# Kernel optimization log

Hardware: AMD Instinct MI355X
Metric: run time of the kernel (lower is better)

Reference implementation:

```python
import jax, jax.numpy as jnp
import numpy as np

V, C, T, H, L, B = 32000, 1024, 1024, 16, 4, 4
HD = C // H
FF = 4 * C
LN_EPS = 1e-5


def _sinusoidal(block_size, n_embd):
    pos = np.arange(block_size, dtype=np.float32)[:, None]
    div = np.exp(np.arange(0, n_embd, 2, dtype=np.float32) * (-np.log(10000.0) / n_embd))
    enc = np.zeros((block_size, n_embd), dtype=np.float32)
    enc[:, 0::2] = np.sin(pos * div)
    enc[:, 1::2] = np.cos(pos * div)
    return jnp.asarray(enc)


def setup_inputs() -> dict:
    key = jax.random.key(0)
    ks = jax.random.split(key, 12)
    std = 0.02
    n = lambda k, s: jax.random.normal(k, s, jnp.float32) * std
    return {
        'idx': jax.random.randint(ks[0], (B, T), 0, V),
        'emb': n(ks[1], (V, C)),
        'pos_enc': _sinusoidal(T, C),
        'Wq': n(ks[2], (L, C, C)),
        'Wk': n(ks[3], (L, C, C)),
        'Wv': n(ks[4], (L, C, C)),
        'Wo': n(ks[5], (L, C, C)),
        'bo': jnp.zeros((L, C), jnp.float32),
        'W1': n(ks[6], (L, C, FF)),
        'b1': jnp.zeros((L, FF), jnp.float32),
        'W2': n(ks[7], (L, FF, C)),
        'b2': jnp.zeros((L, C), jnp.float32),
        'ln1_g': jnp.ones((L, C), jnp.float32),
        'ln1_b': jnp.zeros((L, C), jnp.float32),
        'ln2_g': jnp.ones((L, C), jnp.float32),
        'ln2_b': jnp.zeros((L, C), jnp.float32),
        'lnf_g': jnp.ones((C,), jnp.float32),
        'lnf_b': jnp.zeros((C,), jnp.float32),
        'Wlm': n(ks[8], (C, V)),
        'blm': jnp.zeros((V,), jnp.float32),
    }


def _layer_norm(x, g, b):
    m = jnp.mean(x, -1, keepdims=True)
    v = jnp.var(x, -1, keepdims=True)
    return (x - m) * jax.lax.rsqrt(v + LN_EPS) * g + b


def _forward(idx, emb, pos_enc, Wq, Wk, Wv, Wo, bo, W1, b1, W2, b2,
             ln1_g, ln1_b, ln2_g, ln2_b, lnf_g, lnf_b, Wlm, blm):
    Bv, Tv = idx.shape
    x = emb[idx] + pos_enc[None, :Tv, :]  # [B,T,C]
    mask = jnp.tril(jnp.ones((Tv, Tv), dtype=bool))
    scale = HD ** -0.5

    def block(x, p):
        wq, wk, wv, wo, bov, w1, b1v, w2, b2v, g1, bn1, g2, bn2 = p
        h = _layer_norm(x, g1, bn1)
        q = jnp.einsum('btc,chd->bhtd', h, wq.reshape(C, H, HD))
        k = jnp.einsum('btc,chd->bhtd', h, wk.reshape(C, H, HD))
        v = jnp.einsum('btc,chd->bhtd', h, wv.reshape(C, H, HD))
        wei = jnp.einsum('bhqd,bhkd->bhqk', q, k) * scale
        wei = jnp.where(mask, wei, -jnp.inf)
        wei = jax.nn.softmax(wei, axis=-1)
        o = jnp.einsum('bhqk,bhkd->bhqd', wei, v)
        o = o.transpose(0, 2, 1, 3).reshape(Bv, Tv, C)
        x = x + o @ wo + bov
        h2 = _layer_norm(x, g2, bn2)
        x = x + jax.nn.gelu(h2 @ w1 + b1v, approximate=False) @ w2 + b2v
        return x, None

    x, _ = jax.lax.scan(block, x, (Wq, Wk, Wv, Wo, bo, W1, b1, W2, b2,
                                   ln1_g, ln1_b, ln2_g, ln2_b))
    x = _layer_norm(x, lnf_g, lnf_b)
    return x @ Wlm + blm  # [B,T,V]


def reference(idx, emb, pos_enc, Wq, Wk, Wv, Wo, bo, W1, b1, W2, b2,
              ln1_g, ln1_b, ln2_g, ln2_b, lnf_g, lnf_b, Wlm, blm):
    return _forward(idx, emb, pos_enc, Wq, Wk, Wv, Wo, bo, W1, b1, W2, b2,
                    ln1_g, ln1_b, ln2_g, ln2_b, lnf_g, lnf_b, Wlm, blm)
```

## Files before the change

kernel.cpp:

```cpp
#include <hip/hip_runtime.h>

#define V_  32000
#define C_  1024
#define T_  1024
#define H_  16
#define L_  4
#define B_  4
#define HD_ 64
#define FF_ 4096
#define M_  (B_ * T_)

typedef __attribute__((ext_vector_type(8))) short bf16x8;
typedef __attribute__((ext_vector_type(4))) float f32x4;
typedef unsigned short u16;

#define FENCE() asm volatile("" ::: "memory")
#define BAR()  do { FENCE(); __builtin_amdgcn_s_barrier(); FENCE(); } while (0)
#define VMW(n) asm volatile("s_waitcnt vmcnt(" #n ")" ::: "memory")

__device__ __forceinline__ u16 f2bf(float f) {
  unsigned u = __builtin_bit_cast(unsigned, f);
  u += 0x7fffu + ((u >> 16) & 1u);
  return (u16)(u >> 16);
}

__device__ __forceinline__ float gelu_f(float v) {
  return 0.5f * v * (1.0f + erff(v * 0.70710678118654752f));
}

__device__ __forceinline__ void gload16(const u16* g, u16* l) {
  __builtin_amdgcn_global_load_lds(
      (const __attribute__((address_space(1))) void*)g,
      (__attribute__((address_space(3))) void*)l, 16, 0, 0);
}

template <int FUSE_LN>
__global__ __launch_bounds__(256)
void embed_kernel(const int* __restrict__ idx, const float* __restrict__ emb,
                  const float* __restrict__ pos, float* __restrict__ x,
                  const float* __restrict__ g, const float* __restrict__ bta,
                  u16* __restrict__ hout) {
  int row = blockIdx.x;
  int t = row & (T_ - 1);
  int tok = idx[row];
  float4 e = reinterpret_cast<const float4*>(emb + (size_t)tok * C_)[threadIdx.x];
  float4 p = reinterpret_cast<const float4*>(pos + (size_t)t * C_)[threadIdx.x];
  float4 r;
  r.x = e.x + p.x; r.y = e.y + p.y; r.z = e.z + p.z; r.w = e.w + p.w;
  reinterpret_cast<float4*>(x + (size_t)row * C_)[threadIdx.x] = r;
  if constexpr (FUSE_LN) {
    int tid = threadIdx.x;
    float s  = r.x + r.y + r.z + r.w;
    float ss = r.x * r.x + r.y * r.y + r.z * r.z + r.w * r.w;
    #pragma unroll
    for (int d = 1; d < 64; d <<= 1) {
      s  += __shfl_xor(s, d, 64);
      ss += __shfl_xor(ss, d, 64);
    }
    __shared__ float rs[4], rss[4];
    int w = tid >> 6, lane = tid & 63;
    if (lane == 0) { rs[w] = s; rss[w] = ss; }
    __syncthreads();
    s  = rs[0] + rs[1] + rs[2] + rs[3];
    ss = rss[0] + rss[1] + rss[2] + rss[3];
    float mean = s * (1.0f / C_);
    float var  = ss * (1.0f / C_) - mean * mean;
    float rstd = rsqrtf(var + 1e-5f);
    float4 gv = reinterpret_cast<const float4*>(g)[tid];
    float4 bv = reinterpret_cast<const float4*>(bta)[tid];
    union { u16 u[4]; uint2 v; } pk;
    pk.u[0] = f2bf((r.x - mean) * rstd * gv.x + bv.x);
    pk.u[1] = f2bf((r.y - mean) * rstd * gv.y + bv.y);
    pk.u[2] = f2bf((r.z - mean) * rstd * gv.z + bv.z);
    pk.u[3] = f2bf((r.w - mean) * rstd * gv.w + bv.w);
    *reinterpret_cast<uint2*>(&hout[(size_t)row * C_ + tid * 4]) = pk.v;
  }
}

__global__ __launch_bounds__(256)
void ln_kernel(const float* __restrict__ xin, const float* __restrict__ g,
               const float* __restrict__ bta, u16* __restrict__ out) {
  const int w = threadIdx.x >> 6, lane = threadIdx.x & 63;
  const int row = blockIdx.x * 4 + w;
  const float4* xr = reinterpret_cast<const float4*>(xin + (size_t)row * C_);
  float4 xv[4];
  float s = 0.f, ss = 0.f;
  #pragma unroll
  for (int j = 0; j < 4; ++j) {
    xv[j] = xr[lane + 64 * j];
    s  += xv[j].x + xv[j].y + xv[j].z + xv[j].w;
    ss += xv[j].x * xv[j].x + xv[j].y * xv[j].y + xv[j].z * xv[j].z + xv[j].w * xv[j].w;
  }
  #pragma unroll
  for (int d = 1; d < 64; d <<= 1) {
    s  += __shfl_xor(s, d, 64);
    ss += __shfl_xor(ss, d, 64);
  }
  float mean = s * (1.0f / C_);
  float var  = ss * (1.0f / C_) - mean * mean;
  float rstd = rsqrtf(var + 1e-5f);
  #pragma unroll
  for (int j = 0; j < 4; ++j) {
    float4 gv = reinterpret_cast<const float4*>(g)[lane + 64 * j];
    float4 bv = reinterpret_cast<const float4*>(bta)[lane + 64 * j];
    union { u16 u[4]; uint2 v; } pk;
    pk.u[0] = f2bf((xv[j].x - mean) * rstd * gv.x + bv.x);
    pk.u[1] = f2bf((xv[j].y - mean) * rstd * gv.y + bv.y);
    pk.u[2] = f2bf((xv[j].z - mean) * rstd * gv.z + bv.z);
    pk.u[3] = f2bf((xv[j].w - mean) * rstd * gv.w + bv.w);
    *reinterpret_cast<uint2*>(&out[(size_t)row * C_ + (lane + 64 * j) * 4]) = pk.v;
  }
}

__global__ __launch_bounds__(256)
void wtrans_kernel(const float* __restrict__ W, u16* __restrict__ Wt, int K, int N,
                   size_t dstBS) {
  const float* src = W + (size_t)blockIdx.z * K * N;
  u16* dst = Wt + (size_t)blockIdx.z * dstBS;
  __shared__ float tile[32][33];
  int k0 = blockIdx.y * 32, n0 = blockIdx.x * 32;
  int tx = threadIdx.x & 31, ty = threadIdx.x >> 5;
  #pragma unroll
  for (int i = 0; i < 4; ++i)
    tile[ty * 4 + i][tx] = src[(size_t)(k0 + ty * 4 + i) * N + n0 + tx];
  __syncthreads();
  int n = threadIdx.x >> 3, q = threadIdx.x & 7;
  union { u16 u[4]; uint2 v; } pk;
  #pragma unroll
  for (int j = 0; j < 4; ++j) pk.u[j] = f2bf(tile[4 * q + j][n]);
  *reinterpret_cast<uint2*>(&dst[(size_t)(n0 + n) * K + k0 + 4 * q]) = pk.v;
}

__global__ __launch_bounds__(256)
void wtrans4_kernel(const float* __restrict__ Wq, const float* __restrict__ Wk,
                    const float* __restrict__ Wv, const float* __restrict__ Wo,
                    u16* __restrict__ WqkvT, u16* __restrict__ WoT) {
  int zz = blockIdx.z;
  int l = zz & 3, which = zz >> 2;
  const float* src = (which == 0 ? Wq : which == 1 ? Wk : which == 2 ? Wv : Wo)
                     + (size_t)l * C_ * C_;
  u16* dst = (which == 3)
      ? WoT + (size_t)l * C_ * C_
      : WqkvT + (size_t)l * 3 * C_ * C_ + (size_t)which * C_ * C_;
  __shared__ float tile[32][33];
  int k0 = blockIdx.y * 32, n0 = blockIdx.x * 32;
  int tx = threadIdx.x & 31, ty = threadIdx.x >> 5;
  #pragma unroll
  for (int i = 0; i < 4; ++i)
    tile[ty * 4 + i][tx] = src[(size_t)(k0 + ty * 4 + i) * C_ + n0 + tx];
  __syncthreads();
  int n = threadIdx.x >> 3, q = threadIdx.x & 7;
  union { u16 u[4]; uint2 v; } pk;
  #pragma unroll
  for (int j = 0; j < 4; ++j) pk.u[j] = f2bf(tile[4 * q + j][n]);
  *reinterpret_cast<uint2*>(&dst[(size_t)(n0 + n) * C_ + k0 + 4 * q]) = pk.v;
}

template <int MODE, int GROUP_M>
__global__ __launch_bounds__(256)
void gemm_bt(const u16* __restrict__ A, const u16* __restrict__ Bt,
             const float* __restrict__ bias, const float* __restrict__ resid,
             void* __restrict__ Cout, u16* __restrict__ vtb,
             int M, int N, int K) {
  __shared__ u16 smem[6][4096];
  const int nbm = M >> 7, nbn = N >> 7;
  const int nwg = nbm * nbn;
  const int bid = blockIdx.x;
  const int chunk = nwg >> 3;
  const int swz = (bid & 7) * chunk + (bid >> 3);
  const int gsz = GROUP_M * nbn;
  const int grp = swz / gsz, rem = swz % gsz;
  const int by = grp * GROUP_M + (rem % GROUP_M);
  const int bx = rem / GROUP_M;
  const int m0 = by * 128, n0 = bx * 128;

  const int tid = threadIdx.x, lane = tid & 63, w = tid >> 6;
  const int wr = w >> 1, wc = w & 1;
  const int frow = lane & 15, fk = (lane >> 4) * 8;
  const int srow = lane >> 2, scol = (lane & 3) * 8;

  f32x4 acc[4][4];
  #pragma unroll
  for (int i = 0; i < 4; ++i)
    #pragma unroll
    for (int j = 0; j < 4; ++j) acc[i][j] = (f32x4)0.0f;

  auto stage = [&](int d, int k0) {
    gload16(&A [(size_t)(m0 + w * 32 +      srow) * K + k0 + scol], smem[d] + w * 1024);
    gload16(&A [(size_t)(m0 + w * 32 + 16 + srow) * K + k0 + scol], smem[d] + w * 1024 + 512);
    gload16(&Bt[(size_t)(n0 + w * 32 +      srow) * K + k0 + scol], smem[3 + d] + w * 1024);
    gload16(&Bt[(size_t)(n0 + w * 32 + 16 + srow) * K + k0 + scol], smem[3 + d] + w * 1024 + 512);
  };

  const int NT = K >> 5;
  stage(0, 0); stage(1, 32); stage(2, 64);

  int cur = 0;
  for (int kt = 0; kt < NT; ++kt) {
    if (kt + 3 <= NT)      { VMW(8); }
    else if (kt + 2 == NT) { VMW(4); }
    else                   { VMW(0); }
    BAR();

    bf16x8 af[4], bfr[4];
    #pragma unroll
    for (int mi = 0; mi < 4; ++mi)
      af[mi] = *reinterpret_cast<const bf16x8*>(&smem[cur][(wr * 64 + mi * 16 + frow) * 32 + fk]);
    #pragma unroll
    for (int ni = 0; ni < 4; ++ni)
      bfr[ni] = *reinterpret_cast<const bf16x8*>(&smem[3 + cur][(wc * 64 + ni * 16 + frow) * 32 + fk]);
    #pragma unroll
    for (int mi = 0; mi < 4; ++mi)
      #pragma unroll
      for (int ni = 0; ni < 4; ++ni)
        acc[mi][ni] = __builtin_amdgcn_mfma_f32_16x16x32_bf16(af[mi], bfr[ni], acc[mi][ni], 0, 0, 0);

    BAR();
    if (kt + 3 < NT) stage(cur, (kt + 3) << 5);
    cur = (cur == 2) ? 0 : cur + 1;
  }

  u16* outb = (u16*)Cout;
  float* outf = (float*)Cout;

  if constexpr (MODE == 1) {
    char* ef = (char*)smem;
    #pragma unroll
    for (int h = 0; h < 2; ++h) {
      if (wr == h) {
        #pragma unroll
        for (int mi = 0; mi < 4; ++mi)
          #pragma unroll
          for (int ni = 0; ni < 4; ++ni) {
            int rl0 = mi * 16 + ((lane >> 4) << 2);
            int cl = wc * 64 + ni * 16 + (lane & 15);
            #pragma unroll
            for (int r = 0; r < 4; ++r) {
              int rl = rl0 + r;
              *(float*)(ef + rl * 512 + ((cl * 4) ^ ((rl & 7) << 4))) = acc[mi][ni][r];
            }
          }
      }
      BAR();
      {
        int row = tid >> 2;
        int s = (row & 7) << 4;
        #pragma unroll
        for (int j = 0; j < 8; ++j) {
          int g = (tid & 3) + 4 * j;
          float4 v = *reinterpret_cast<float4*>(ef + row * 512 + ((g * 16) ^ s));
          int ocol = n0 + g * 4;
          float4 bv4 = *reinterpret_cast<const float4*>(&bias[ocol]);
          size_t off = (size_t)(m0 + h * 64 + row) * N + ocol;
          float4 rv = *reinterpret_cast<const float4*>(&resid[off]);
          float4 o;
          o.x = v.x + bv4.x + rv.x; o.y = v.y + bv4.y + rv.y;
          o.z = v.z + bv4.z + rv.z; o.w = v.w + bv4.w + rv.w;
          *reinterpret_cast<float4*>(&outf[off]) = o;
        }
      }
      BAR();
    }
    return;
  }

  if constexpr (MODE == 4) {
    const bool vblk = (n0 >= 2 * C_);
    if (!vblk) {
      char* ef = (char*)smem;
      #pragma unroll
      for (int mi = 0; mi < 4; ++mi)
        #pragma unroll
        for (int ni = 0; ni < 4; ++ni) {
          int rl0 = wr * 64 + mi * 16 + ((lane >> 4) << 2);
          int cl = wc * 64 + ni * 16 + (lane & 15);
          #pragma unroll
          for (int r = 0; r < 4; ++r) {
            int rl = rl0 + r;
            *(u16*)(ef + rl * 256 + ((cl * 2) ^ ((rl & 7) << 4))) = f2bf(acc[mi][ni][r]);
          }
        }
      BAR();
      int cc = tid & 15;
      #pragma unroll
      for (int j = 0; j < 8; ++j) {
        int rr = (tid >> 4) + 16 * j;
        uint4 v = *reinterpret_cast<uint4*>(ef + rr * 256 + ((cc * 16) ^ ((rr & 7) << 4)));
        *reinterpret_cast<uint4*>(&outb[(size_t)(m0 + rr) * (2 * C_) + n0 + cc * 8]) = v;
      }
    } else {
      #pragma unroll
      for (int mi = 0; mi < 4; ++mi)
        #pragma unroll
        for (int ni = 0; ni < 4; ++ni) {
          int orow = m0 + wr * 64 + mi * 16 + ((lane >> 4) << 2);
          int ocol = n0 + wc * 64 + ni * 16 + (lane & 15);
          int vcol = ocol - 2 * C_;
          int hh = vcol >> 6, d = vcol & 63;
          int bb = orow >> 10, t0 = orow & (T_ - 1);
          union { u16 u[4]; uint2 v2; } pk;
          #pragma unroll
          for (int r = 0; r < 4; ++r) pk.u[r] = f2bf(acc[mi][ni][r]);
          *reinterpret_cast<uint2*>(
              &vtb[(((size_t)bb * H_ + hh) * HD_ + d) * T_ + t0]) = pk.v2;
        }
    }
    return;
  }

  #pragma unroll
  for (int mi = 0; mi < 4; ++mi) {
    #pragma unroll
    for (int ni = 0; ni < 4; ++ni) {
      int orow = m0 + wr * 64 + mi * 16 + ((lane >> 4) << 2);
      int ocol = n0 + wc * 64 + ni * 16 + (lane & 15);
      float bv = 0.0f;
      if constexpr (MODE == 2 || MODE == 3) bv = bias[ocol];
      #pragma unroll
      for (int r = 0; r < 4; ++r) {
        size_t off = (size_t)(orow + r) * N + ocol;
        float val = acc[mi][ni][r] + bv;
        if constexpr (MODE == 0) {
          outb[off] = f2bf(val);
        } else if constexpr (MODE == 2) {
          outb[off] = f2bf(gelu_f(val));
        } else if constexpr (MODE == 3) {
          outf[off] = val;
        }
      }
    }
  }
}

template <int MODE>
__global__ __launch_bounds__(512, 2)
void gemm8(const u16* __restrict__ A, const u16* __restrict__ Bt,
           const float* __restrict__ bias, const float* __restrict__ resid,
           void* __restrict__ Cout, int M, int N, int K) {
  __shared__ u16 lds8[65536];
  const int nbm = M >> 8, nbn = N >> 8;
  const int nwg = nbm * nbn;
  const int chunk = nwg >> 3;
  const int bid = blockIdx.x;
  const int swz = (bid & 7) * chunk + (bid >> 3);
  const int gsz = 4 * nbn;
  const int grp = swz / gsz, rem = swz % gsz;
  const int by = grp * 4 + (rem & 3);
  const int bx = rem >> 2;
  const int m0 = by << 8, n0 = bx << 8;

  const int tid = threadIdx.x, lane = tid & 63, w = tid >> 6;
  const int wm = w >> 2, wn = w & 3;
  const int fr = lane & 15, kgb = (lane >> 4) * 16;
  const int scolz = 8 * ((lane & 7) ^ (lane >> 3));
  const int NT = K >> 6;
  const int NI = NT >> 1;

  f32x4 acc[8][4];
  #pragma unroll
  for (int i = 0; i < 8; ++i)
    #pragma unroll
    for (int j = 0; j < 4; ++j) acc[i][j] = (f32x4)0.0f;

  auto ldr = [&](int d, int isB, int row, int cb) -> bf16x8 {
    int bo = row * 128 + (cb ^ ((row & 7) << 4));
    const char* base = (const char*)lds8 + d * 65536 + isB * 32768 +
                       (isB ? (wn >> 1) : wm) * 16384;
    return *reinterpret_cast<const bf16x8*>(base + bo);
  };
  auto stage_half = [&](const u16* grow0, u16* ldst) {
    #pragma unroll
    for (int p = 0; p < 2; ++p) {
      int r = (p * 8 + w) * 8 + (lane >> 3);
      gload16(grow0 + (size_t)r * K + scolz, ldst + (p * 8 + w) * 512);
    }
  };
  auto stageA = [&](int d, int h, int t) {
    stage_half(&A[(size_t)(m0 + h * 128) * K + t * 64],
               lds8 + d * 32768 + h * 8192);
  };
  auto stageB = [&](int d, int h, int t) {
    stage_half(&Bt[(size_t)(n0 + h * 128) * K + t * 64],
               lds8 + d * 32768 + 16384 + h * 8192);
  };

  bf16x8 af[2][2], bfr[4][2];

#define LDA_Q(d, q) do {                                   \
    af[0][0] = ldr(d, 0, (q) * 32 + fr,      kgb);         \
    af[0][1] = ldr(d, 0, (q) * 32 + fr,      64 + kgb);    \
    af[1][0] = ldr(d, 0, (q) * 32 + 16 + fr, kgb);         \
    af[1][1] = ldr(d, 0, (q) * 32 + 16 + fr, 64 + kgb);    \
  } while (0)
#define LDB_ALL(d) do {                                    \
    _Pragma("unroll")                                      \
    for (int nj = 0; nj < 4; ++nj) {                       \
      bfr[nj][0] = ldr(d, 1, (wn & 1) * 64 + nj * 16 + fr, kgb);      \
      bfr[nj][1] = ldr(d, 1, (wn & 1) * 64 + nj * 16 + fr, 64 + kgb); \
    }                                                      \
  } while (0)
#define MFMA_Q(q) do {                                     \
    __builtin_amdgcn_s_setprio(1);                         \
    _Pragma("unroll")                                      \
    for (int lmi = 0; lmi < 2; ++lmi)                      \
      _Pragma("unroll")                                    \
      for (int nj = 0; nj < 4; ++nj)                       \
        _Pragma("unroll")                                  \
        for (int ks = 0; ks < 2; ++ks)                     \
          acc[2 * (q) + lmi][nj] = __builtin_amdgcn_mfma_f32_16x16x32_bf16( \
              af[lmi][ks], bfr[nj][ks], acc[2 * (q) + lmi][nj], 0, 0, 0);   \
    __builtin_amdgcn_s_setprio(0);                         \
  } while (0)

  stageB(0, 0, 0); stageB(0, 1, 0);
  stageA(0, 0, 0); stageA(0, 1, 0);
  stageB(1, 0, 1); stageB(1, 1, 1);
  VMW(4);
  BAR();

  for (int i = 0; i < NI; ++i) {
    const int a = 2 * i, b = 2 * i + 1;
    const bool pa = (a + 2 < NT), pb = (b + 2 < NT);
    LDB_ALL(0); LDA_Q(0, 0);
    stageA(1, 0, b);
    BAR(); MFMA_Q(0); BAR();
    LDA_Q(0, 1);
    stageA(1, 1, b);
    if (pa) stageB(0, 0, a + 2);
    BAR(); MFMA_Q(1); BAR();
    LDA_Q(0, 2);
    if (pa) stageB(0, 1, a + 2);
    BAR(); MFMA_Q(2); BAR();
    LDA_Q(0, 3);
    BAR(); MFMA_Q(3);
    if (pa) { VMW(4); } else { VMW(0); }
    BAR();
    LDB_ALL(1); LDA_Q(1, 0);
    if (pa) stageA(0, 0, a + 2);
    BAR(); MFMA_Q(0); BAR();
    LDA_Q(1, 1);
    if (pa) stageA(0, 1, a + 2);
    BAR(); MFMA_Q(1); BAR();
    LDA_Q(1, 2);
    if (pb) stageB(1, 0, b + 2);
    BAR(); MFMA_Q(2); BAR();
    LDA_Q(1, 3);
    if (pb) stageB(1, 1, b + 2);
    BAR(); MFMA_Q(3);
    if (pb) { VMW(4); } else { VMW(0); }
    BAR();
  }
#undef LDA_Q
#undef LDB_ALL
#undef MFMA_Q

  u16* outb = (u16*)Cout;
  float* outf = (float*)Cout;
  #pragma unroll
  for (int mi = 0; mi < 8; ++mi) {
    #pragma unroll
    for (int nj = 0; nj < 4; ++nj) {
      int orow = m0 + wm * 128 + mi * 16 + ((lane >> 4) << 2);
      int ocol = n0 + wn * 64 + nj * 16 + (lane & 15);
      float bv = 0.0f;
      if constexpr (MODE != 0) bv = bias[ocol];
      #pragma unroll
      for (int r = 0; r < 4; ++r) {
        size_t off = (size_t)(orow + r) * N + ocol;
        float val = acc[mi][nj][r] + bv;
        if constexpr (MODE == 0) {
          outb[off] = f2bf(val);
        } else if constexpr (MODE == 1) {
          outf[off] = val + resid[off];
        } else if constexpr (MODE == 2) {
          outb[off] = f2bf(gelu_f(val));
        } else {
          outf[off] = val;
        }
      }
    }
  }
}

template <int MODE>
__global__ __launch_bounds__(256)
void gemm_legacy(const u16* __restrict__ A, const float* __restrict__ Bw,
                 const float* __restrict__ bias, const float* __restrict__ resid,
                 void* __restrict__ Cout, int M, int N, int K) {
  __shared__ u16 As[128][40];
  __shared__ u16 Bs[128][40];
  const int m0 = blockIdx.y * 128, n0 = blockIdx.x * 128;
  const int tid = threadIdx.x, lane = tid & 63, w = tid >> 6;
  const int wr = w >> 1, wc = w & 1;
  const int row = lane & 15, kk8 = (lane >> 4) * 8;
  f32x4 acc[4][4];
  #pragma unroll
  for (int i = 0; i < 4; ++i)
    #pragma unroll
    for (int j = 0; j < 4; ++j) acc[i][j] = (f32x4)0.0f;
  for (int k0 = 0; k0 < K; k0 += 32) {
    #pragma unroll
    for (int i = 0; i < 2; ++i) {
      int e = (tid + i * 256) * 8;
      int r = e >> 5, c = e & 31;
      *reinterpret_cast<uint4*>(&As[r][c]) =
        *reinterpret_cast<const uint4*>(&A[(size_t)(m0 + r) * K + k0 + c]);
    }
    #pragma unroll
    for (int i = 0; i < 4; ++i) {
      int e = (tid + i * 256) * 4;
      int kr = e >> 7, c = e & 127;
      float4 bv = *reinterpret_cast<const float4*>(&Bw[(size_t)(k0 + kr) * N + n0 + c]);
      Bs[c + 0][kr] = f2bf(bv.x);
      Bs[c + 1][kr] = f2bf(bv.y);
      Bs[c + 2][kr] = f2bf(bv.z);
      Bs[c + 3][kr] = f2bf(bv.w);
    }
    __syncthreads();
    bf16x8 af[4], bfr[4];
    #pragma unroll
    for (int mi = 0; mi < 4; ++mi)
      af[mi] = *reinterpret_cast<const bf16x8*>(&As[wr * 64 + mi * 16 + row][kk8]);
    #pragma unroll
    for (int ni = 0; ni < 4; ++ni)
      bfr[ni] = *reinterpret_cast<const bf16x8*>(&Bs[wc * 64 + ni * 16 + row][kk8]);
    #pragma unroll
    for (int mi = 0; mi < 4; ++mi)
      #pragma unroll
      for (int ni = 0; ni < 4; ++ni)
        acc[mi][ni] = __builtin_amdgcn_mfma_f32_16x16x32_bf16(af[mi], bfr[ni], acc[mi][ni], 0, 0, 0);
    __syncthreads();
  }
  u16* outb = (u16*)Cout;
  float* outf = (float*)Cout;
  #pragma unroll
  for (int mi = 0; mi < 4; ++mi) {
    #pragma unroll
    for (int ni = 0; ni < 4; ++ni) {
      int orow = m0 + wr * 64 + mi * 16 + ((lane >> 4) << 2);
      int ocol = n0 + wc * 64 + ni * 16 + (lane & 15);
      float bv = 0.0f;
      if constexpr (MODE != 0) bv = bias[ocol];
      #pragma unroll
      for (int r = 0; r < 4; ++r) {
        size_t off = (size_t)(orow + r) * N + ocol;
        float val = acc[mi][ni][r] + bv;
        if constexpr (MODE == 0) outb[off] = f2bf(val);
        else if constexpr (MODE == 1) outf[off] = val + resid[off];
        else if constexpr (MODE == 2) {
          outb[off] = f2bf(gelu_f(val));
        } else outf[off] = val;
      }
    }
  }
}

__global__ __launch_bounds__(512)
void attn_kernel(const u16* __restrict__ qg, const u16* __restrict__ kg,
                 const u16* __restrict__ vt, u16* __restrict__ og) {
  const int bh = blockIdx.y;
  const int q0 = blockIdx.x * 128;
  const int b = bh >> 4;
  const int tid = threadIdx.x, lane = tid & 63, w = tid >> 6;
  const int fr = lane & 15, kk8 = (lane >> 4) * 8;
  __shared__ u16 KS[2][4096];
  __shared__ u16 VS[2][4096];
  __shared__ u16 Ps[8][16][72];

  const int ldq = 2 * C_;
  const size_t baseq = ((size_t)b * T_) * ldq + (bh & 15) * HD_;
  const u16* qbase = qg + baseq;
  const u16* kbase = kg + baseq;
  const u16* vbase = vt + ((size_t)bh * HD_) * T_;
  const size_t baseo = ((size_t)b * T_) * C_ + (bh & 15) * HD_;
  const int qw = q0 + w * 16;

  bf16x8 qf[2];
  #pragma unroll
  for (int s = 0; s < 2; ++s)
    qf[s] = *reinterpret_cast<const bf16x8*>(&qbase[(size_t)(qw + fr) * ldq + s * 32 + kk8]);

  const int srow8 = lane >> 3;
  const int scol = 8 * ((lane & 7) ^ srow8);
  auto stageKV = [&](int d, int kv0) {
    int rr = w * 8 + srow8;
    gload16(kbase + (size_t)(kv0 + rr) * ldq + scol, &KS[d][w * 512]);
    gload16(vbase + (size_t)rr * T_ + kv0 + scol,    &VS[d][w * 512]);
  };
  auto ldS = [&](const u16* base, int row, int cu) -> bf16x8 {
    return *reinterpret_cast<const bf16x8*>(&base[row * 64 + (cu ^ ((row & 7) << 3))]);
  };

  f32x4 acc_o[4];
  #pragma unroll
  for (int dt = 0; dt < 4; ++dt) acc_o[dt] = (f32x4)0.0f;
  float m_run[4] = {-1e30f, -1e30f, -1e30f, -1e30f};
  float l_run[4] = {0.f, 0.f, 0.f, 0.f};
  const float scale = 0.125f;

  const int kv_end = q0 + 128;
  stageKV(0, 0);
  VMW(0); BAR();

  int cur = 0;
  for (int kv0 = 0; kv0 < kv_end; kv0 += 64, cur ^= 1) {
    if (kv0 + 64 < kv_end) stageKV(cur ^ 1, kv0 + 64);

    f32x4 sacc[4];
    #pragma unroll
    for (int nt = 0; nt < 4; ++nt) sacc[nt] = (f32x4)0.0f;
    #pragma unroll
    for (int nt = 0; nt < 4; ++nt)
      #pragma unroll
      for (int s = 0; s < 2; ++s) {
        bf16x8 kf = ldS(KS[cur], nt * 16 + fr, s * 32 + kk8);
        sacc[nt] = __builtin_amdgcn_mfma_f32_16x16x32_bf16(qf[s], kf, sacc[nt], 0, 0, 0);
      }

    #pragma unroll
    for (int i = 0; i < 4; ++i) {
      int qrow = qw + ((lane >> 4) << 2) + i;
      float sv[4], pv[4];
      #pragma unroll
      for (int nt = 0; nt < 4; ++nt) {
        sv[nt] = sacc[nt][i] * scale;
        if (kv0 + nt * 16 + (lane & 15) > qrow) sv[nt] = -1e30f;
      }
      float mx = fmaxf(fmaxf(sv[0], sv[1]), fmaxf(sv[2], sv[3]));
      #pragma unroll
      for (int d = 1; d < 16; d <<= 1) mx = fmaxf(mx, __shfl_xor(mx, d, 64));
      float mnew = fmaxf(m_run[i], mx);
      float rsum = 0.0f;
      #pragma unroll
      for (int nt = 0; nt < 4; ++nt) { pv[nt] = __expf(sv[nt] - mnew); rsum += pv[nt]; }
      float alpha = __expf(m_run[i] - mnew);
      #pragma unroll
      for (int d = 1; d < 16; d <<= 1) rsum += __shfl_xor(rsum, d, 64);
      l_run[i] = l_run[i] * alpha + rsum;
      m_run[i] = mnew;
      #pragma unroll
      for (int dt = 0; dt < 4; ++dt) acc_o[dt][i] *= alpha;
      #pragma unroll
      for (int nt = 0; nt < 4; ++nt)
        Ps[w][((lane >> 4) << 2) + i][(lane & 15) + nt * 16] = f2bf(pv[nt]);
    }

    #pragma unroll
    for (int dt = 0; dt < 4; ++dt)
      #pragma unroll
      for (int s = 0; s < 2; ++s) {
        bf16x8 pf = *reinterpret_cast<const bf16x8*>(&Ps[w][fr][s * 32 + kk8]);
        bf16x8 vf = ldS(VS[cur], dt * 16 + fr, s * 32 + kk8);
        acc_o[dt] = __builtin_amdgcn_mfma_f32_16x16x32_bf16(pf, vf, acc_o[dt], 0, 0, 0);
      }
    VMW(0); BAR();
  }

  #pragma unroll
  for (int dt = 0; dt < 4; ++dt)
    #pragma unroll
    for (int i = 0; i < 4; ++i) {
      int r = qw + ((lane >> 4) << 2) + i;
      float val = acc_o[dt][i] / l_run[i];
      og[baseo + (size_t)r * C_ + dt * 16 + (lane & 15)] = f2bf(val);
    }
}

__global__ __launch_bounds__(256)
void attn_legacy(const u16* __restrict__ qg, const u16* __restrict__ kg,
                 const u16* __restrict__ vg, u16* __restrict__ og, int ldq) {
  const int bh = blockIdx.y;
  const int b = bh >> 4, hh = bh & 15;
  const int q0 = blockIdx.x * 64;
  const int tid = threadIdx.x, lane = tid & 63, w = tid >> 6;
  const int row = lane & 15, kk8 = (lane >> 4) * 8;
  __shared__ u16 Ks[64][72];
  __shared__ u16 Vt[64][72];
  __shared__ u16 Ps[4][16][72];

  const size_t basei = ((size_t)b * T_) * ldq + hh * HD_;
  const size_t baseo = ((size_t)b * T_) * C_ + hh * HD_;
  const int qw = q0 + w * 16;

  bf16x8 qf[2];
  #pragma unroll
  for (int s = 0; s < 2; ++s)
    qf[s] = *reinterpret_cast<const bf16x8*>(&qg[basei + (size_t)(qw + row) * ldq + s * 32 + kk8]);

  f32x4 acc_o[4];
  #pragma unroll
  for (int dt = 0; dt < 4; ++dt) acc_o[dt] = (f32x4)0.0f;
  float m_run[4] = {-1e30f, -1e30f, -1e30f, -1e30f};
  float l_run[4] = {0.f, 0.f, 0.f, 0.f};
  const float scale = 0.125f;

  const int sc = (tid & 7) * 8;
  const int kv_end = q0 + 64;
  for (int kv0 = 0; kv0 < kv_end; kv0 += 64) {
    #pragma unroll
    for (int p = 0; p < 2; ++p) {
      int sr = p * 32 + (tid >> 3);
      *reinterpret_cast<uint4*>(&Ks[sr][sc]) =
        *reinterpret_cast<const uint4*>(&kg[basei + (size_t)(kv0 + sr) * ldq + sc]);
      union { uint4 u4; u16 us[8]; } vv;
      vv.u4 = *reinterpret_cast<const uint4*>(&vg[basei + (size_t)(kv0 + sr) * ldq + sc]);
      #pragma unroll
      for (int j = 0; j < 8; ++j) Vt[sc + j][sr] = vv.us[j];
    }
    __syncthreads();

    f32x4 sacc[4];
    #pragma unroll
    for (int nt = 0; nt < 4; ++nt) sacc[nt] = (f32x4)0.0f;
    #pragma unroll
    for (int nt = 0; nt < 4; ++nt)
      #pragma unroll
      for (int s = 0; s < 2; ++s) {
        bf16x8 kf = *reinterpret_cast<const bf16x8*>(&Ks[nt * 16 + row][s * 32 + kk8]);
        sacc[nt] = __builtin_amdgcn_mfma_f32_16x16x32_bf16(qf[s], kf, sacc[nt], 0, 0, 0);
      }

    #pragma unroll
    for (int i = 0; i < 4; ++i) {
      int qrow = qw + ((lane >> 4) << 2) + i;
      float sv[4], pv[4];
      #pragma unroll
      for (int nt = 0; nt < 4; ++nt) {
        sv[nt] = sacc[nt][i] * scale;
        if (kv0 + nt * 16 + (lane & 15) > qrow) sv[nt] = -1e30f;
      }
      float mx = fmaxf(fmaxf(sv[0], sv[1]), fmaxf(sv[2], sv[3]));
      #pragma unroll
      for (int d = 1; d < 16; d <<= 1) mx = fmaxf(mx, __shfl_xor(mx, d, 64));
      float mnew = fmaxf(m_run[i], mx);
      float rsum = 0.0f;
      #pragma unroll
      for (int nt = 0; nt < 4; ++nt) { pv[nt] = __expf(sv[nt] - mnew); rsum += pv[nt]; }
      float alpha = __expf(m_run[i] - mnew);
      #pragma unroll
      for (int d = 1; d < 16; d <<= 1) rsum += __shfl_xor(rsum, d, 64);
      l_run[i] = l_run[i] * alpha + rsum;
      m_run[i] = mnew;
      #pragma unroll
      for (int nt = 0; nt < 4; ++nt)
        Ps[w][((lane >> 4) << 2) + i][(lane & 15) + nt * 16] = f2bf(pv[nt]);
      #pragma unroll
      for (int dt = 0; dt < 4; ++dt) acc_o[dt][i] *= alpha;
    }

    #pragma unroll
    for (int dt = 0; dt < 4; ++dt)
      #pragma unroll
      for (int s = 0; s < 2; ++s) {
        bf16x8 pf = *reinterpret_cast<const bf16x8*>(&Ps[w][row][s * 32 + kk8]);
        bf16x8 vf = *reinterpret_cast<const bf16x8*>(&Vt[dt * 16 + row][s * 32 + kk8]);
        acc_o[dt] = __builtin_amdgcn_mfma_f32_16x16x32_bf16(pf, vf, acc_o[dt], 0, 0, 0);
      }
    __syncthreads();
  }

  #pragma unroll
  for (int dt = 0; dt < 4; ++dt)
    #pragma unroll
    for (int i = 0; i < 4; ++i) {
      int r = qw + ((lane >> 4) << 2) + i;
      float val = acc_o[dt][i] / l_run[i];
      og[baseo + (size_t)r * C_ + dt * 16 + (lane & 15)] = f2bf(val);
    }
}

extern "C" void kernel_launch(void* const* d_in, const int* in_sizes, int n_in,
                              void* d_out, int out_size, void* d_ws, size_t ws_size,
                              hipStream_t stream) {
  const int*   idx  = (const int*)d_in[0];
  const float* emb  = (const float*)d_in[1];
  const float* pos  = (const float*)d_in[2];
  const float* Wq   = (const float*)d_in[3];
  const float* Wk   = (const float*)d_in[4];
  const float* Wv   = (const float*)d_in[5];
  const float* Wo   = (const float*)d_in[6];
  const float* bo   = (const float*)d_in[7];
  const float* W1   = (const float*)d_in[8];
  const float* b1   = (const float*)d_in[9];
  const float* W2   = (const float*)d_in[10];
  const float* b2   = (const float*)d_in[11];
  const float* ln1g = (const float*)d_in[12];
  const float* ln1b = (const float*)d_in[13];
  const float* ln2g = (const float*)d_in[14];
  const float* ln2b = (const float*)d_in[15];
  const float* lnfg = (const float*)d_in[16];
  const float* lnfb = (const float*)d_in[17];
  const float* Wlm  = (const float*)d_in[18];
  const float* blm  = (const float*)d_in[19];

  char* ws = (char*)d_ws;
  float* x    = (float*)ws;
  u16*   h    = (u16*)(ws + (16u << 20));
  u16*   qkv  = (u16*)(ws + (24u << 20));
  u16*   vtb  = (u16*)(ws + (40u << 20));
  u16*   ob   = (u16*)(ws + (48u << 20));
  u16*   ffb  = (u16*)(ws + (24u << 20));

  u16* WqkvT = (u16*)(ws + (56u  << 20));
  u16* WoT   = (u16*)(ws + (80u  << 20));
  u16* W1T   = (u16*)(ws + (88u  << 20));
  u16* W2T   = (u16*)(ws + (120u << 20));
  u16* WlmT  = (u16*)(ws + (152u << 20));
  const size_t WS_NEED = (152ull << 20) + 2ull * C_ * V_;

  dim3 blk(256), blk8(512), blkA(512);
  const int nQKV = (M_ / 128) * (3 * C_ / 128);
  const int nCC  = (M_ / 128) * (C_ / 128);
  const int nF1_8 = (M_ / 256) * (FF_ / 256);
  const int nLM_8 = (M_ / 256) * (V_ / 256);
  dim3 gA(T_ / 128, B_ * H_);

  if (ws_size >= WS_NEED) {
    const size_t s3 = (size_t)3 * C_ * C_;
    embed_kernel<1><<<M_, blk, 0, stream>>>(idx, emb, pos, x, ln1g, ln1b, h);
    wtrans4_kernel<<<dim3(C_ / 32, C_ / 32, 16), blk, 0, stream>>>(Wq, Wk, Wv, Wo, WqkvT, WoT);
    wtrans_kernel<<<dim3(FF_ / 32, C_ / 32, L_), blk, 0, stream>>>(W1, W1T, C_, FF_, (size_t)C_ * FF_);
    wtrans_kernel<<<dim3(C_ / 32, FF_ / 32, L_), blk, 0, stream>>>(W2, W2T, FF_, C_, (size_t)C_ * FF_);
    wtrans_kernel<<<dim3(V_ / 32,  C_ / 32, 1),  blk, 0, stream>>>(Wlm, WlmT, C_, V_, (size_t)C_ * V_);

    for (int l = 0; l < L_; ++l) {
      if (l > 0)
        ln_kernel<<<M_ / 4, blk, 0, stream>>>(x, ln1g + l * C_, ln1b + l * C_, h);
      gemm_bt<4, 8><<<nQKV, blk, 0, stream>>>(h, WqkvT + (size_t)l * s3, nullptr, nullptr, qkv, vtb, M_, 3 * C_, C_);
      attn_kernel<<<gA, blkA, 0, stream>>>(qkv, qkv + C_, vtb, ob);
      gemm_bt<1, 8><<<nCC, blk, 0, stream>>>(ob, WoT + (size_t)l * C_ * C_, bo + l * C_, x, x, nullptr, M_, C_, C_);
      ln_kernel<<<M_ / 4, blk, 0, stream>>>(x, ln2g + l * C_, ln2b + l * C_, h);
      gemm8<2><<<nF1_8, blk8, 0, stream>>>(h, W1T + (size_t)l * C_ * FF_, b1 + l * FF_, nullptr, ffb, M_, FF_, C_);
      gemm_bt<1, 8><<<nCC, blk, 0, stream>>>(ffb, W2T + (size_t)l * C_ * FF_, b2 + l * C_, x, x, nullptr, M_, C_, FF_);
    }
    ln_kernel<<<M_ / 4, blk, 0, stream>>>(x, lnfg, lnfb, h);
    gemm8<3><<<nLM_8, blk8, 0, stream>>>(h, WlmT, blm, nullptr, (float*)d_out, M_, V_, C_);
  } else {
    embed_kernel<0><<<M_, blk, 0, stream>>>(idx, emb, pos, x, nullptr, nullptr, nullptr);
    float* xr = x;
    u16* qb = qkv;
    u16* kb = qkv + (size_t)M_ * C_;
    u16* vb = (u16*)(ws + (40u << 20));
    dim3 gC(C_ / 128, M_ / 128);
    dim3 gF(FF_ / 128, M_ / 128);
    dim3 gV(V_ / 128, M_ / 128);
    dim3 gAl(T_ / 64, B_ * H_);
    for (int l = 0; l < L_; ++l) {
      ln_kernel<<<M_ / 4, blk, 0, stream>>>(xr, ln1g + l * C_, ln1b + l * C_, h);
      gemm_legacy<0><<<gC, blk, 0, stream>>>(h, Wq + (size_t)l * C_ * C_, nullptr, nullptr, qb, M_, C_, C_);
      gemm_legacy<0><<<gC, blk, 0, stream>>>(h, Wk + (size_t)l * C_ * C_, nullptr, nullptr, kb, M_, C_, C_);
      gemm_legacy<0><<<gC, blk, 0, stream>>>(h, Wv + (size_t)l * C_ * C_, nullptr, nullptr, vb, M_, C_, C_);
      attn_legacy<<<gAl, blk, 0, stream>>>(qb, kb, vb, ob, C_);
      gemm_legacy<1><<<gC, blk, 0, stream>>>(ob, Wo + (size_t)l * C_ * C_, bo + l * C_, xr, xr, M_, C_, C_);
      ln_kernel<<<M_ / 4, blk, 0, stream>>>(xr, ln2g + l * C_, ln2b + l * C_, h);
      gemm_legacy<2><<<gF, blk, 0, stream>>>(h, W1 + (size_t)l * C_ * FF_, b1 + l * FF_, nullptr, ffb, M_, FF_, C_);
      gemm_legacy<1><<<gC, blk, 0, stream>>>(ffb, W2 + (size_t)l * FF_ * C_, b2 + l * C_, xr, xr, M_, C_, FF_);
    }
    ln_kernel<<<M_ / 4, blk, 0, stream>>>(xr, lnfg, lnfb, h);
    gemm_legacy<3><<<gV, blk, 0, stream>>>(h, Wlm, blm, nullptr, (float*)d_out, M_, V_, C_);
  }
}
```

Measured before the change: 1.355 ms.

## Replace 256x256 gemm8 kernel with 128-tile gemm_bt for FFN1 and LM head

Removes the 512-thread 256x256-tile gemm8 kernel and routes the FFN up-projection and LM-head GEMMs through the 128x128-tile gemm_bt kernel. It also adds an LDS-staged epilogue for the GELU mode, so bf16 outputs go out as 16-byte vector stores. The smaller tiles give more workgroups and may help balance or occupancy, at the cost of less operand reuse per tile and the loss of gemm8's hand-tuned pipeline.

```diff
diff --git a/kernel.cpp b/kernel.cpp
--- a/kernel.cpp
+++ b/kernel.cpp
@@ -264,6 +264,32 @@
     return;
   }
 
+  if constexpr (MODE == 2) {
+    char* ef = (char*)smem;
+    #pragma unroll
+    for (int mi = 0; mi < 4; ++mi)
+      #pragma unroll
+      for (int ni = 0; ni < 4; ++ni) {
+        int rl0 = wr * 64 + mi * 16 + ((lane >> 4) << 2);
+        int cl = wc * 64 + ni * 16 + (lane & 15);
+        float bv = bias[n0 + cl];
+        #pragma unroll
+        for (int r = 0; r < 4; ++r) {
+          int rl = rl0 + r;
+          *(u16*)(ef + rl * 256 + ((cl * 2) ^ ((rl & 7) << 4))) = f2bf(gelu_f(acc[mi][ni][r] + bv));
+        }
+      }
+    BAR();
+    int cc = tid & 15;
+    #pragma unroll
+    for (int j = 0; j < 8; ++j) {
+      int rr = (tid >> 4) + 16 * j;
+      uint4 v = *reinterpret_cast<uint4*>(ef + rr * 256 + ((cc * 16) ^ ((rr & 7) << 4)));
+      *reinterpret_cast<uint4*>(&outb[(size_t)(m0 + rr) * N + n0 + cc * 8]) = v;
+    }
+    return;
+  }
+
   if constexpr (MODE == 4) {
     const bool vblk = (n0 >= 2 * C_);
     if (!vblk) {
@@ -315,165 +341,13 @@
       int orow = m0 + wr * 64 + mi * 16 + ((lane >> 4) << 2);
       int ocol = n0 + wc * 64 + ni * 16 + (lane & 15);
       float bv = 0.0f;
-      if constexpr (MODE == 2 || MODE == 3) bv = bias[ocol];
+      if constexpr (MODE == 3) bv = bias[ocol];
       #pragma unroll
       for (int r = 0; r < 4; ++r) {
         size_t off = (size_t)(orow + r) * N + ocol;
         float val = acc[mi][ni][r] + bv;
         if constexpr (MODE == 0) {
           outb[off] = f2bf(val);
-        } else if constexpr (MODE == 2) {
-          outb[off] = f2bf(gelu_f(val));
-        } else if constexpr (MODE == 3) {
-          outf[off] = val;
-        }
-      }
-    }
-  }
-}
-
-template <int MODE>
-__global__ __launch_bounds__(512, 2)
-void gemm8(const u16* __restrict__ A, const u16* __restrict__ Bt,
-           const float* __restrict__ bias, const float* __restrict__ resid,
-           void* __restrict__ Cout, int M, int N, int K) {
-  __shared__ u16 lds8[65536];
-  const int nbm = M >> 8, nbn = N >> 8;
-  const int nwg = nbm * nbn;
-  const int chunk = nwg >> 3;
-  const int bid = blockIdx.x;
-  const int swz = (bid & 7) * chunk + (bid >> 3);
-  const int gsz = 4 * nbn;
-  const int grp = swz / gsz, rem = swz % gsz;
-  const int by = grp * 4 + (rem & 3);
-  const int bx = rem >> 2;
-  const int m0 = by << 8, n0 = bx << 8;
-
-  const int tid = threadIdx.x, lane = tid & 63, w = tid >> 6;
-  const int wm = w >> 2, wn = w & 3;
-  const int fr = lane & 15, kgb = (lane >> 4) * 16;
-  const int scolz = 8 * ((lane & 7) ^ (lane >> 3));
-  const int NT = K >> 6;
-  const int NI = NT >> 1;
-
-  f32x4 acc[8][4];
-  #pragma unroll
-  for (int i = 0; i < 8; ++i)
-    #pragma unroll
-    for (int j = 0; j < 4; ++j) acc[i][j] = (f32x4)0.0f;
-
-  auto ldr = [&](int d, int isB, int row, int cb) -> bf16x8 {
-    int bo = row * 128 + (cb ^ ((row & 7) << 4));
-    const char* base = (const char*)lds8 + d * 65536 + isB * 32768 +
-                       (isB ? (wn >> 1) : wm) * 16384;
-    return *reinterpret_cast<const bf16x8*>(base + bo);
-  };
-  auto stage_half = [&](const u16* grow0, u16* ldst) {
-    #pragma unroll
-    for (int p = 0; p < 2; ++p) {
-      int r = (p * 8 + w) * 8 + (lane >> 3);
-      gload16(grow0 + (size_t)r * K + scolz, ldst + (p * 8 + w) * 512);
-    }
-  };
-  auto stageA = [&](int d, int h, int t) {
-    stage_half(&A[(size_t)(m0 + h * 128) * K + t * 64],
-               lds8 + d * 32768 + h * 8192);
-  };
-  auto stageB = [&](int d, int h, int t) {
-    stage_half(&Bt[(size_t)(n0 + h * 128) * K + t * 64],
-               lds8 + d * 32768 + 16384 + h * 8192);
-  };
-
-  bf16x8 af[2][2], bfr[4][2];
-
-#define LDA_Q(d, q) do {                                   \
-    af[0][0] = ldr(d, 0, (q) * 32 + fr,      kgb);         \
-    af[0][1] = ldr(d, 0, (q) * 32 + fr,      64 + kgb);    \
-    af[1][0] = ldr(d, 0, (q) * 32 + 16 + fr, kgb);         \
-    af[1][1] = ldr(d, 0, (q) * 32 + 16 + fr, 64 + kgb);    \
-  } while (0)
-#define LDB_ALL(d) do {                                    \
-    _Pragma("unroll")                                      \
-    for (int nj = 0; nj < 4; ++nj) {                       \
-      bfr[nj][0] = ldr(d, 1, (wn & 1) * 64 + nj * 16 + fr, kgb);      \
-      bfr[nj][1] = ldr(d, 1, (wn & 1) * 64 + nj * 16 + fr, 64 + kgb); \
-    }                                                      \
-  } while (0)
-#define MFMA_Q(q) do {                                     \
-    __builtin_amdgcn_s_setprio(1);                         \
-    _Pragma("unroll")                                      \
-    for (int lmi = 0; lmi < 2; ++lmi)                      \
-      _Pragma("unroll")                                    \
-      for (int nj = 0; nj < 4; ++nj)                       \
-        _Pragma("unroll")                                  \
-        for (int ks = 0; ks < 2; ++ks)                     \
-          acc[2 * (q) + lmi][nj] = __builtin_amdgcn_mfma_f32_16x16x32_bf16( \
-              af[lmi][ks], bfr[nj][ks], acc[2 * (q) + lmi][nj], 0, 0, 0);   \
-    __builtin_amdgcn_s_setprio(0);                         \
-  } while (0)
-
-  stageB(0, 0, 0); stageB(0, 1, 0);
-  stageA(0, 0, 0); stageA(0, 1, 0);
-  stageB(1, 0, 1); stageB(1, 1, 1);
-  VMW(4);
-  BAR();
-
-  for (int i = 0; i < NI; ++i) {
-    const int a = 2 * i, b = 2 * i + 1;
-    const bool pa = (a + 2 < NT), pb = (b + 2 < NT);
-    LDB_ALL(0); LDA_Q(0, 0);
-    stageA(1, 0, b);
-    BAR(); MFMA_Q(0); BAR();
-    LDA_Q(0, 1);
-    stageA(1, 1, b);
-    if (pa) stageB(0, 0, a + 2);
-    BAR(); MFMA_Q(1); BAR();
-    LDA_Q(0, 2);
-    if (pa) stageB(0, 1, a + 2);
-    BAR(); MFMA_Q(2); BAR();
-    LDA_Q(0, 3);
-    BAR(); MFMA_Q(3);
-    if (pa) { VMW(4); } else { VMW(0); }
-    BAR();
-    LDB_ALL(1); LDA_Q(1, 0);
-    if (pa) stageA(0, 0, a + 2);
-    BAR(); MFMA_Q(0); BAR();
-    LDA_Q(1, 1);
-    if (pa) stageA(0, 1, a + 2);
-    BAR(); MFMA_Q(1); BAR();
-    LDA_Q(1, 2);
-    if (pb) stageB(1, 0, b + 2);
-    BAR(); MFMA_Q(2); BAR();
-    LDA_Q(1, 3);
-    if (pb) stageB(1, 1, b + 2);
-    BAR(); MFMA_Q(3);
-    if (pb) { VMW(4); } else { VMW(0); }
-    BAR();
-  }
-#undef LDA_Q
-#undef LDB_ALL
-#undef MFMA_Q
-
-  u16* outb = (u16*)Cout;
-  float* outf = (float*)Cout;
-  #pragma unroll
-  for (int mi = 0; mi < 8; ++mi) {
-    #pragma unroll
-    for (int nj = 0; nj < 4; ++nj) {
-      int orow = m0 + wm * 128 + mi * 16 + ((lane >> 4) << 2);
-      int ocol = n0 + wn * 64 + nj * 16 + (lane & 15);
-      float bv = 0.0f;
-      if constexpr (MODE != 0) bv = bias[ocol];
-      #pragma unroll
-      for (int r = 0; r < 4; ++r) {
-        size_t off = (size_t)(orow + r) * N + ocol;
-        float val = acc[mi][nj][r] + bv;
-        if constexpr (MODE == 0) {
-          outb[off] = f2bf(val);
-        } else if constexpr (MODE == 1) {
-          outf[off] = val + resid[off];
-        } else if constexpr (MODE == 2) {
-          outb[off] = f2bf(gelu_f(val));
         } else {
           outf[off] = val;
         }
@@ -808,11 +682,11 @@
   u16* WlmT  = (u16*)(ws + (152u << 20));
   const size_t WS_NEED = (152ull << 20) + 2ull * C_ * V_;
 
-  dim3 blk(256), blk8(512), blkA(512);
-  const int nQKV = (M_ / 128) * (3 * C_ / 128);
-  const int nCC  = (M_ / 128) * (C_ / 128);
-  const int nF1_8 = (M_ / 256) * (FF_ / 256);
-  const int nLM_8 = (M_ / 256) * (V_ / 256);
+  dim3 blk(256), blkA(512);
+  const int nQKV  = (M_ / 128) * (3 * C_ / 128);
+  const int nCC   = (M_ / 128) * (C_ / 128);
+  const int nF1   = (M_ / 128) * (FF_ / 128);
+  const int nLM   = (M_ / 128) * (V_ / 128);
   dim3 gA(T_ / 128, B_ * H_);
 
   if (ws_size >= WS_NEED) {
@@ -830,11 +704,11 @@
       attn_kernel<<<gA, blkA, 0, stream>>>(qkv, qkv + C_, vtb, ob);
       gemm_bt<1, 8><<<nCC, blk, 0, stream>>>(ob, WoT + (size_t)l * C_ * C_, bo + l * C_, x, x, nullptr, M_, C_, C_);
       ln_kernel<<<M_ / 4, blk, 0, stream>>>(x, ln2g + l * C_, ln2b + l * C_, h);
-      gemm8<2><<<nF1_8, blk8, 0, stream>>>(h, W1T + (size_t)l * C_ * FF_, b1 + l * FF_, nullptr, ffb, M_, FF_, C_);
+      gemm_bt<2, 8><<<nF1, blk, 0, stream>>>(h, W1T + (size_t)l * C_ * FF_, b1 + l * FF_, nullptr, ffb, nullptr, M_, FF_, C_);
       gemm_bt<1, 8><<<nCC, blk, 0, stream>>>(ffb, W2T + (size_t)l * C_ * FF_, b2 + l * C_, x, x, nullptr, M_, C_, FF_);
     }
     ln_kernel<<<M_ / 4, blk, 0, stream>>>(x, lnfg, lnfb, h);
-    gemm8<3><<<nLM_8, blk8, 0, stream>>>(h, WlmT, blm, nullptr, (float*)d_out, M_, V_, C_);
+    gemm_bt<3, 8><<<nLM, blk, 0, stream>>>(h, WlmT, blm, nullptr, (float*)d_out, nullptr, M_, V_, C_);
   } else {
     embed_kernel<0><<<M_, blk, 0, stream>>>(idx, emb, pos, x, nullptr, nullptr, nullptr);
     float* xr = x;
```

Result: slower. 1.434 ms (+5.8%).
